# Kernel tuning notes

Hardware: AMD Instinct MI355X
Metric: run time of the kernel (lower is better)

The kernel has to match this reference:

```python
import math
import jax, jax.numpy as jnp
import numpy as np

N, NFEAT, NHID, NCLASS, NLAYERS = 8192, 500, 128, 40, 4
ALPHA, GAMMA, LAMBDA, MAX_W = 0.1, 0.1, 0.5, 0.05


def _col_stochastic(w):
    # Uniform(0,1) -> clamp to [0, MAX_W] -> column normalize (ColumnStochasticGraphConvolution init)
    w = jnp.clip(w, 0.0, MAX_W)
    return w / jnp.clip(w.sum(axis=0, keepdims=True), 1e-8, None)


def setup_inputs() -> dict:
    key = jax.random.key(0)
    ks = jax.random.split(key, 10)
    x = jax.random.normal(ks[0], (N, NFEAT), dtype=jnp.float32)
    adj = (jax.random.uniform(ks[1], (N, N)) < 0.002).astype(jnp.float32)
    s_in = 1.0 / math.sqrt(NFEAT)
    fc_in_w = jax.random.uniform(ks[2], (NFEAT, NHID), minval=-s_in, maxval=s_in, dtype=jnp.float32)
    fc_in_b = jnp.zeros((NHID,), jnp.float32)
    c = jax.random.normal(ks[3], (NHID,), dtype=jnp.float32)
    s_h = 1.0 / math.sqrt(NHID)
    w_gcnii = jax.random.uniform(ks[4], (NLAYERS, NHID, NHID), minval=-s_h, maxval=s_h, dtype=jnp.float32)
    b_gcnii = jax.random.uniform(ks[5], (NLAYERS, NHID), minval=-s_h, maxval=s_h, dtype=jnp.float32)
    w_lin = jax.vmap(_col_stochastic)(jax.random.uniform(ks[6], (NLAYERS, NHID, NHID), dtype=jnp.float32))
    b_lin = jnp.zeros((NLAYERS, NHID), jnp.float32)
    fc_out_w = jax.random.uniform(ks[7], (NHID, NCLASS), minval=-s_h, maxval=s_h, dtype=jnp.float32)
    fc_out_b = jnp.zeros((NCLASS,), jnp.float32)
    return {"x": x, "adj": adj, "fc_in_w": fc_in_w, "fc_in_b": fc_in_b, "c": c,
            "w_gcnii": w_gcnii, "b_gcnii": b_gcnii, "w_lin": w_lin, "b_lin": b_lin,
            "fc_out_w": fc_out_w, "fc_out_b": fc_out_b}


def _normalize_adj(adj):
    # A_hat = D^{-1/2} (A + I) D^{-1/2}
    a = adj + jnp.eye(adj.shape[0], dtype=adj.dtype)
    deg = a.sum(axis=1)
    dinv = jnp.where(deg > 0, jax.lax.rsqrt(deg), 0.0)
    return dinv[:, None] * a * dinv[None, :]


def reference(x, adj, fc_in_w, fc_in_b, c, w_gcnii, b_gcnii, w_lin, b_lin, fc_out_w, fc_out_b):
    a_hat = _normalize_adj(adj)                      # [N, N]
    h = jax.nn.relu(x @ fc_in_w + fc_in_b)           # [N, nhid]
    h = (1.0 - GAMMA) * h + GAMMA * c[None, :]       # H0 preconditioning with learnable c
    h0 = h
    # dropout is identity in eval mode
    for i in range(NLAYERS):
        beta = math.log(LAMBDA / (i + 1) + 1.0)
        # linear propagation branch: A_hat @ (H W'_i) + b'_i  (column-stochastic W')
        linear_part = a_hat @ (h @ w_lin[i]) + b_lin[i]
        # GCNII branch: sigma(((1-a) A_hat H + a H0)((1-b) I + b W_i)) + b_i
        support = (1.0 - ALPHA) * (a_hat @ h) + ALPHA * h0
        gcnii = jax.nn.relu((1.0 - beta) * support + beta * (support @ w_gcnii[i]) + b_gcnii[i])
        h = linear_part + gcnii
    return h @ fc_out_w + fc_out_b                   # [N, nclass] logits
```

## Files before the change

### kernel.cpp

```cpp
#include <hip/hip_runtime.h>
#include <math.h>

#define NROWS 8192
#define NFEATD 500
#define NHID 128
#define NCLS 40
#define CAP 64
#define FCIN_BLOCKS (NROWS / 8)
#define CSR_BLOCKS  (NROWS / 4)
#define ROWS_PB 8

typedef float f32x4 __attribute__((ext_vector_type(4)));
typedef float f32x2 __attribute__((ext_vector_type(2)));

__global__ __launch_bounds__(256) void k_pre(
    const float* __restrict__ x, const float* __restrict__ w,
    const float* __restrict__ b, const float* __restrict__ c,
    const float* __restrict__ adj,
    float* __restrict__ h, float* __restrict__ h0,
    float* __restrict__ dinv, int* __restrict__ cnts, int* __restrict__ cols)
{
    __shared__ float xs[8][504];
    int tid = threadIdx.x;
    if (blockIdx.x < FCIN_BLOCKS) {
        int col = tid & 127;
        int rg = tid >> 7;
        int r0 = blockIdx.x * 8;
        for (int rr = 0; rr < 8; ++rr)
            for (int k = tid; k < NFEATD; k += 256)
                xs[rr][k] = x[(size_t)(r0 + rr) * NFEATD + k];
        __syncthreads();
        float bias = b[col];
        float acc[4] = {bias, bias, bias, bias};
        for (int k4 = 0; k4 < NFEATD / 4; ++k4) {
            int k = k4 * 4;
            f32x4 a0 = *(const f32x4*)&xs[rg * 4 + 0][k];
            f32x4 a1 = *(const f32x4*)&xs[rg * 4 + 1][k];
            f32x4 a2 = *(const f32x4*)&xs[rg * 4 + 2][k];
            f32x4 a3 = *(const f32x4*)&xs[rg * 4 + 3][k];
            float w0 = w[(k + 0) * NHID + col];
            float w1 = w[(k + 1) * NHID + col];
            float w2 = w[(k + 2) * NHID + col];
            float w3 = w[(k + 3) * NHID + col];
            acc[0] += a0.x * w0 + a0.y * w1 + a0.z * w2 + a0.w * w3;
            acc[1] += a1.x * w0 + a1.y * w1 + a1.z * w2 + a1.w * w3;
            acc[2] += a2.x * w0 + a2.y * w1 + a2.z * w2 + a2.w * w3;
            acc[3] += a3.x * w0 + a3.y * w1 + a3.z * w2 + a3.w * w3;
        }
        float cv = c[col];
#pragma unroll
        for (int rr = 0; rr < 4; ++rr) {
            float hv = 0.9f * fmaxf(acc[rr], 0.0f) + 0.1f * cv;
            size_t o = (size_t)(r0 + rg * 4 + rr) * NHID + col;
            h[o] = hv;
            h0[o] = hv;
        }
    } else {
        int bid = blockIdx.x - FCIN_BLOCKS;
        int r = bid * 4 + (tid >> 6);
        int lane = tid & 63;
        const f32x4* row4 = (const f32x4*)(adj + (size_t)r * NROWS);
        int* mycols = cols + (size_t)r * CAP;
        unsigned long long lt = (1ull << lane) - 1ull;
        int cnt = 0;
        for (int it = 0; it < NROWS / 256; ++it) {
            f32x4 v = __builtin_nontemporal_load(&row4[it * 64 + lane]);
            int base = it * 256 + 4 * lane;
            bool nz; unsigned long long m;
            nz = (v.x != 0.0f); m = __ballot(nz);
            if (nz) { int p = cnt + __popcll(m & lt); mycols[p < CAP ? p : CAP - 1] = base; }
            cnt += __popcll(m);
            nz = (v.y != 0.0f); m = __ballot(nz);
            if (nz) { int p = cnt + __popcll(m & lt); mycols[p < CAP ? p : CAP - 1] = base + 1; }
            cnt += __popcll(m);
            nz = (v.z != 0.0f); m = __ballot(nz);
            if (nz) { int p = cnt + __popcll(m & lt); mycols[p < CAP ? p : CAP - 1] = base + 2; }
            cnt += __popcll(m);
            nz = (v.w != 0.0f); m = __ballot(nz);
            if (nz) { int p = cnt + __popcll(m & lt); mycols[p < CAP ? p : CAP - 1] = base + 3; }
            cnt += __popcll(m);
        }
        if (lane == 0) {
            cnts[r] = cnt < CAP ? cnt : CAP;
            dinv[r] = rsqrtf((float)cnt + 1.0f);
        }
    }
}

__global__ __launch_bounds__(256) void k_scale(
    const float* __restrict__ h, const float* __restrict__ dinv,
    float* __restrict__ ht)
{
    int gid = blockIdx.x * 256 + threadIdx.x;
    float2 v = ((const float2*)h)[gid];
    float d = dinv[gid >> 6];
    ((float2*)ht)[gid] = make_float2(v.x * d, v.y * d);
}

__global__ __launch_bounds__(256) void k_layer(
    const float* __restrict__ ht, const float* __restrict__ h0,
    const float* __restrict__ dinv, const int* __restrict__ cnts,
    const int* __restrict__ cols,
    const float* __restrict__ wlin, const float* __restrict__ blin,
    const float* __restrict__ wg, const float* __restrict__ bg,
    float beta, float* __restrict__ htout,
    const float* __restrict__ fow, const float* __restrict__ fob,
    float* __restrict__ out, int final_layer)
{
    __shared__ float ahs[ROWS_PB][NHID];
    __shared__ float ss[ROWS_PB][NHID];
    __shared__ float red[2][ROWS_PB][NHID];
    int tid = threadIdx.x;
    int lane = tid & 63;
    int wid = tid >> 6;
    int r0 = blockIdx.x * ROWS_PB;
    const float2* ht2 = (const float2*)ht;
    const float2* h02 = (const float2*)h0;

    for (int rr = 2 * wid; rr < 2 * wid + 2; ++rr) {
        int r = r0 + rr;
        int n = cnts[r];
        const int* mc = cols + (size_t)r * CAP;
        float ax = 0.f, ay = 0.f;
        int e = 0;
        for (; e + 4 <= n; e += 4) {
            int j0 = mc[e], j1 = mc[e + 1], j2 = mc[e + 2], j3 = mc[e + 3];
            float2 v0 = ht2[(size_t)j0 * 64 + lane];
            float2 v1 = ht2[(size_t)j1 * 64 + lane];
            float2 v2 = ht2[(size_t)j2 * 64 + lane];
            float2 v3 = ht2[(size_t)j3 * 64 + lane];
            ax += v0.x + v1.x + v2.x + v3.x;
            ay += v0.y + v1.y + v2.y + v3.y;
        }
        for (; e < n; ++e) {
            int j = mc[e];
            float2 v = ht2[(size_t)j * 64 + lane];
            ax += v.x;
            ay += v.y;
        }
        float di = dinv[r];
        float2 ti = ht2[(size_t)r * 64 + lane];
        float gx = di * (ax + ti.x);
        float gy = di * (ay + ti.y);
        float2 h0v = h02[(size_t)r * 64 + lane];
        ((float2*)&ahs[rr][0])[lane] = make_float2(gx, gy);
        ((float2*)&ss[rr][0])[lane] =
            make_float2(0.9f * gx + 0.1f * h0v.x, 0.9f * gy + 0.1f * h0v.y);
    }
    __syncthreads();

    int br = tid >> 7;
    int kh = (tid >> 6) & 1;
    int cp = tid & 63;
    const float* wmat = br ? wg : wlin;
    const float (*amat)[NHID] = br ? ss : ahs;
    f32x2 acc[8] = {{0,0},{0,0},{0,0},{0,0},{0,0},{0,0},{0,0},{0,0}};
    int kbase = kh * 64;
    for (int k4 = 0; k4 < 16; ++k4) {
        int k = kbase + 4 * k4;
        f32x4 a0 = *(const f32x4*)&amat[0][k];
        f32x4 a1 = *(const f32x4*)&amat[1][k];
        f32x4 a2 = *(const f32x4*)&amat[2][k];
        f32x4 a3 = *(const f32x4*)&amat[3][k];
        f32x4 a4 = *(const f32x4*)&amat[4][k];
        f32x4 a5 = *(const f32x4*)&amat[5][k];
        f32x4 a6 = *(const f32x4*)&amat[6][k];
        f32x4 a7 = *(const f32x4*)&amat[7][k];
        f32x2 w0 = ((const f32x2*)&wmat[(size_t)(k + 0) * NHID])[cp];
        f32x2 w1 = ((const f32x2*)&wmat[(size_t)(k + 1) * NHID])[cp];
        f32x2 w2 = ((const f32x2*)&wmat[(size_t)(k + 2) * NHID])[cp];
        f32x2 w3 = ((const f32x2*)&wmat[(size_t)(k + 3) * NHID])[cp];
        acc[0] += a0.x * w0 + a0.y * w1 + a0.z * w2 + a0.w * w3;
        acc[1] += a1.x * w0 + a1.y * w1 + a1.z * w2 + a1.w * w3;
        acc[2] += a2.x * w0 + a2.y * w1 + a2.z * w2 + a2.w * w3;
        acc[3] += a3.x * w0 + a3.y * w1 + a3.z * w2 + a3.w * w3;
        acc[4] += a4.x * w0 + a4.y * w1 + a4.z * w2 + a4.w * w3;
        acc[5] += a5.x * w0 + a5.y * w1 + a5.z * w2 + a5.w * w3;
        acc[6] += a6.x * w0 + a6.y * w1 + a6.z * w2 + a6.w * w3;
        acc[7] += a7.x * w0 + a7.y * w1 + a7.z * w2 + a7.w * w3;
    }

    if (kh == 1) {
#pragma unroll
        for (int rr = 0; rr < 8; ++rr)
            ((f32x2*)&red[br][rr][0])[cp] = acc[rr];
    }
    __syncthreads();
    if (kh == 0) {
#pragma unroll
        for (int rr = 0; rr < 8; ++rr)
            acc[rr] += ((const f32x2*)&red[br][rr][0])[cp];
    }
    f32x2 gv[8];
    if (br == 1 && kh == 0) {
        f32x2 bgv = ((const f32x2*)bg)[cp];
        float omb = 1.0f - beta;
#pragma unroll
        for (int rr = 0; rr < 8; ++rr) {
            f32x2 sv = ((const f32x2*)&ss[rr][0])[cp];
            f32x2 t = omb * sv + beta * acc[rr] + bgv;
            gv[rr].x = fmaxf(t.x, 0.f);
            gv[rr].y = fmaxf(t.y, 0.f);
        }
    }
    __syncthreads();
    if (br == 1 && kh == 0) {
#pragma unroll
        for (int rr = 0; rr < 8; ++rr)
            ((f32x2*)&red[0][rr][0])[cp] = gv[rr];
    }
    __syncthreads();

    if (!final_layer) {
        if (br == 0 && kh == 0) {
            f32x2 blv = ((const f32x2*)blin)[cp];
#pragma unroll
            for (int rr = 0; rr < 8; ++rr) {
                int row = r0 + rr;
                f32x2 g = ((const f32x2*)&red[0][rr][0])[cp];
                f32x2 o = acc[rr] + blv + g;
                ((f32x2*)htout)[(size_t)row * 64 + cp] = dinv[row] * o;
            }
        }
    } else {
        if (br == 0 && kh == 0) {
            f32x2 blv = ((const f32x2*)blin)[cp];
#pragma unroll
            for (int rr = 0; rr < 8; ++rr) {
                f32x2 g = ((const f32x2*)&red[0][rr][0])[cp];
                ((f32x2*)&ss[rr][0])[cp] = acc[rr] + blv + g;
            }
        }
        __syncthreads();
        int rr2 = tid >> 6, c2 = tid & 63;
        if (c2 < NCLS) {
#pragma unroll
            for (int half = 0; half < 2; ++half) {
                int lr = half * 4 + rr2;
                float a = fob[c2];
                for (int k = 0; k < NHID; ++k)
                    a += ss[lr][k] * fow[k * NCLS + c2];
                out[(size_t)(r0 + lr) * NCLS + c2] = a;
            }
        }
    }
}

extern "C" void kernel_launch(void* const* d_in, const int* in_sizes, int n_in,
                              void* d_out, int out_size, void* d_ws, size_t ws_size,
                              hipStream_t stream) {
    const float* x        = (const float*)d_in[0];
    const float* adj      = (const float*)d_in[1];
    const float* fc_in_w  = (const float*)d_in[2];
    const float* fc_in_b  = (const float*)d_in[3];
    const float* c        = (const float*)d_in[4];
    const float* w_gcnii  = (const float*)d_in[5];
    const float* b_gcnii  = (const float*)d_in[6];
    const float* w_lin    = (const float*)d_in[7];
    const float* b_lin    = (const float*)d_in[8];
    const float* fc_out_w = (const float*)d_in[9];
    const float* fc_out_b = (const float*)d_in[10];
    float* out = (float*)d_out;

    char* ws = (char*)d_ws;
    size_t off = 0;
    auto alloc = [&](size_t bytes) -> void* {
        void* p = ws + off;
        off += (bytes + 255) & ~(size_t)255;
        return p;
    };
    float* dinv = (float*)alloc((size_t)NROWS * 4);
    int*   cnts = (int*)  alloc((size_t)NROWS * 4);
    int*   cols = (int*)  alloc((size_t)NROWS * CAP * 4);
    float* hA   = (float*)alloc((size_t)NROWS * NHID * 4);
    float* h0   = (float*)alloc((size_t)NROWS * NHID * 4);
    float* htA  = (float*)alloc((size_t)NROWS * NHID * 4);
    float* htB  = (float*)alloc((size_t)NROWS * NHID * 4);

    k_pre<<<FCIN_BLOCKS + CSR_BLOCKS, 256, 0, stream>>>(
        x, fc_in_w, fc_in_b, c, adj, hA, h0, dinv, cnts, cols);
    k_scale<<<NROWS * 64 / 256, 256, 0, stream>>>(hA, dinv, htA);

    float* htb[2] = {htA, htB};
    for (int i = 0; i < 4; ++i) {
        float beta = logf(0.5f / (float)(i + 1) + 1.0f);
        k_layer<<<NROWS / ROWS_PB, 256, 0, stream>>>(
            htb[i & 1], h0, dinv, cnts, cols,
            w_lin + (size_t)i * NHID * NHID, b_lin + (size_t)i * NHID,
            w_gcnii + (size_t)i * NHID * NHID, b_gcnii + (size_t)i * NHID,
            beta, htb[(i + 1) & 1],
            fc_out_w, fc_out_b, out, (i == 3) ? 1 : 0);
    }
}
```

Baseline: 186.2 us.

## Fuse dinv prescale into first layer and widen layer blocks to 512 threads

Removes the separate k_scale kernel. The first layer now applies dinv per edge while it gathers unscaled h, which drops one launch and one full read and write of the hidden matrix. The layer kernel moves to 512 threads, so each wave gathers a single row and the K dimension of the dense matmul is split four ways with a three-buffer shared-memory reduction. The cost is extra shared memory, more reduction work, and per-edge dinv loads in layer 0.

Result: slower. 198.8 us (+6.7%).

```diff
diff --git a/kernel.cpp b/kernel.cpp
--- a/kernel.cpp
+++ b/kernel.cpp
@@ -87,76 +87,91 @@
     }
 }
 
-__global__ __launch_bounds__(256) void k_scale(
-    const float* __restrict__ h, const float* __restrict__ dinv,
-    float* __restrict__ ht)
-{
-    int gid = blockIdx.x * 256 + threadIdx.x;
-    float2 v = ((const float2*)h)[gid];
-    float d = dinv[gid >> 6];
-    ((float2*)ht)[gid] = make_float2(v.x * d, v.y * d);
-}
-
-__global__ __launch_bounds__(256) void k_layer(
-    const float* __restrict__ ht, const float* __restrict__ h0,
+__global__ __launch_bounds__(512) void k_layer(
+    const float* __restrict__ hin, const float* __restrict__ h0,
     const float* __restrict__ dinv, const int* __restrict__ cnts,
     const int* __restrict__ cols,
     const float* __restrict__ wlin, const float* __restrict__ blin,
     const float* __restrict__ wg, const float* __restrict__ bg,
     float beta, float* __restrict__ htout,
     const float* __restrict__ fow, const float* __restrict__ fob,
-    float* __restrict__ out, int final_layer)
+    float* __restrict__ out, int edge_dinv, int final_layer)
 {
     __shared__ float ahs[ROWS_PB][NHID];
     __shared__ float ss[ROWS_PB][NHID];
-    __shared__ float red[2][ROWS_PB][NHID];
+    __shared__ float red[3][2][ROWS_PB][NHID];
     int tid = threadIdx.x;
     int lane = tid & 63;
     int wid = tid >> 6;
     int r0 = blockIdx.x * ROWS_PB;
-    const float2* ht2 = (const float2*)ht;
+    const float2* h2 = (const float2*)hin;
     const float2* h02 = (const float2*)h0;
 
-    for (int rr = 2 * wid; rr < 2 * wid + 2; ++rr) {
+    {
+        int rr = wid;
         int r = r0 + rr;
         int n = cnts[r];
         const int* mc = cols + (size_t)r * CAP;
         float ax = 0.f, ay = 0.f;
         int e = 0;
-        for (; e + 4 <= n; e += 4) {
-            int j0 = mc[e], j1 = mc[e + 1], j2 = mc[e + 2], j3 = mc[e + 3];
-            float2 v0 = ht2[(size_t)j0 * 64 + lane];
-            float2 v1 = ht2[(size_t)j1 * 64 + lane];
-            float2 v2 = ht2[(size_t)j2 * 64 + lane];
-            float2 v3 = ht2[(size_t)j3 * 64 + lane];
-            ax += v0.x + v1.x + v2.x + v3.x;
-            ay += v0.y + v1.y + v2.y + v3.y;
-        }
-        for (; e < n; ++e) {
-            int j = mc[e];
-            float2 v = ht2[(size_t)j * 64 + lane];
-            ax += v.x;
-            ay += v.y;
-        }
-        float di = dinv[r];
-        float2 ti = ht2[(size_t)r * 64 + lane];
-        float gx = di * (ax + ti.x);
-        float gy = di * (ay + ti.y);
+        if (edge_dinv) {
+            for (; e + 4 <= n; e += 4) {
+                int j0 = mc[e], j1 = mc[e + 1], j2 = mc[e + 2], j3 = mc[e + 3];
+                float d0 = dinv[j0], d1 = dinv[j1], d2 = dinv[j2], d3 = dinv[j3];
+                float2 v0 = h2[(size_t)j0 * 64 + lane];
+                float2 v1 = h2[(size_t)j1 * 64 + lane];
+                float2 v2 = h2[(size_t)j2 * 64 + lane];
+                float2 v3 = h2[(size_t)j3 * 64 + lane];
+                ax += d0 * v0.x + d1 * v1.x + d2 * v2.x + d3 * v3.x;
+                ay += d0 * v0.y + d1 * v1.y + d2 * v2.y + d3 * v3.y;
+            }
+            for (; e < n; ++e) {
+                int j = mc[e];
+                float dj = dinv[j];
+                float2 v = h2[(size_t)j * 64 + lane];
+                ax += dj * v.x;
+                ay += dj * v.y;
+            }
+            float di = dinv[r];
+            float2 vi = h2[(size_t)r * 64 + lane];
+            ax = di * (ax + di * vi.x);
+            ay = di * (ay + di * vi.y);
+        } else {
+            for (; e + 4 <= n; e += 4) {
+                int j0 = mc[e], j1 = mc[e + 1], j2 = mc[e + 2], j3 = mc[e + 3];
+                float2 v0 = h2[(size_t)j0 * 64 + lane];
+                float2 v1 = h2[(size_t)j1 * 64 + lane];
+                float2 v2 = h2[(size_t)j2 * 64 + lane];
+                float2 v3 = h2[(size_t)j3 * 64 + lane];
+                ax += v0.x + v1.x + v2.x + v3.x;
+                ay += v0.y + v1.y + v2.y + v3.y;
+            }
+            for (; e < n; ++e) {
+                int j = mc[e];
+                float2 v = h2[(size_t)j * 64 + lane];
+                ax += v.x;
+                ay += v.y;
+            }
+            float di = dinv[r];
+            float2 ti = h2[(size_t)r * 64 + lane];
+            ax = di * (ax + ti.x);
+            ay = di * (ay + ti.y);
+        }
         float2 h0v = h02[(size_t)r * 64 + lane];
-        ((float2*)&ahs[rr][0])[lane] = make_float2(gx, gy);
+        ((float2*)&ahs[rr][0])[lane] = make_float2(ax, ay);
         ((float2*)&ss[rr][0])[lane] =
-            make_float2(0.9f * gx + 0.1f * h0v.x, 0.9f * gy + 0.1f * h0v.y);
+            make_float2(0.9f * ax + 0.1f * h0v.x, 0.9f * ay + 0.1f * h0v.y);
     }
     __syncthreads();
 
-    int br = tid >> 7;
-    int kh = (tid >> 6) & 1;
+    int br = tid >> 8;
+    int kq = (tid >> 6) & 3;
     int cp = tid & 63;
     const float* wmat = br ? wg : wlin;
     const float (*amat)[NHID] = br ? ss : ahs;
     f32x2 acc[8] = {{0,0},{0,0},{0,0},{0,0},{0,0},{0,0},{0,0},{0,0}};
-    int kbase = kh * 64;
-    for (int k4 = 0; k4 < 16; ++k4) {
+    int kbase = kq * 32;
+    for (int k4 = 0; k4 < 8; ++k4) {
         int k = kbase + 4 * k4;
         f32x4 a0 = *(const f32x4*)&amat[0][k];
         f32x4 a1 = *(const f32x4*)&amat[1][k];
@@ -180,19 +195,23 @@
         acc[7] += a7.x * w0 + a7.y * w1 + a7.z * w2 + a7.w * w3;
     }
 
-    if (kh == 1) {
+    if (kq != 0) {
 #pragma unroll
         for (int rr = 0; rr < 8; ++rr)
-            ((f32x2*)&red[br][rr][0])[cp] = acc[rr];
+            ((f32x2*)&red[kq - 1][br][rr][0])[cp] = acc[rr];
     }
     __syncthreads();
-    if (kh == 0) {
-#pragma unroll
-        for (int rr = 0; rr < 8; ++rr)
-            acc[rr] += ((const f32x2*)&red[br][rr][0])[cp];
+    if (kq == 0) {
+#pragma unroll
+        for (int rr = 0; rr < 8; ++rr) {
+            f32x2 p0 = ((const f32x2*)&red[0][br][rr][0])[cp];
+            f32x2 p1 = ((const f32x2*)&red[1][br][rr][0])[cp];
+            f32x2 p2 = ((const f32x2*)&red[2][br][rr][0])[cp];
+            acc[rr] += p0 + p1 + p2;
+        }
     }
     f32x2 gv[8];
-    if (br == 1 && kh == 0) {
+    if (br == 1 && kq == 0) {
         f32x2 bgv = ((const f32x2*)bg)[cp];
         float omb = 1.0f - beta;
 #pragma unroll
@@ -204,44 +223,40 @@
         }
     }
     __syncthreads();
-    if (br == 1 && kh == 0) {
+    if (br == 1 && kq == 0) {
 #pragma unroll
         for (int rr = 0; rr < 8; ++rr)
-            ((f32x2*)&red[0][rr][0])[cp] = gv[rr];
+            ((f32x2*)&red[0][0][rr][0])[cp] = gv[rr];
     }
     __syncthreads();
 
     if (!final_layer) {
-        if (br == 0 && kh == 0) {
+        if (br == 0 && kq == 0) {
             f32x2 blv = ((const f32x2*)blin)[cp];
 #pragma unroll
             for (int rr = 0; rr < 8; ++rr) {
                 int row = r0 + rr;
-                f32x2 g = ((const f32x2*)&red[0][rr][0])[cp];
+                f32x2 g = ((const f32x2*)&red[0][0][rr][0])[cp];
                 f32x2 o = acc[rr] + blv + g;
                 ((f32x2*)htout)[(size_t)row * 64 + cp] = dinv[row] * o;
             }
         }
     } else {
-        if (br == 0 && kh == 0) {
+        if (br == 0 && kq == 0) {
             f32x2 blv = ((const f32x2*)blin)[cp];
 #pragma unroll
             for (int rr = 0; rr < 8; ++rr) {
-                f32x2 g = ((const f32x2*)&red[0][rr][0])[cp];
+                f32x2 g = ((const f32x2*)&red[0][0][rr][0])[cp];
                 ((f32x2*)&ss[rr][0])[cp] = acc[rr] + blv + g;
             }
         }
         __syncthreads();
         int rr2 = tid >> 6, c2 = tid & 63;
         if (c2 < NCLS) {
-#pragma unroll
-            for (int half = 0; half < 2; ++half) {
-                int lr = half * 4 + rr2;
-                float a = fob[c2];
-                for (int k = 0; k < NHID; ++k)
-                    a += ss[lr][k] * fow[k * NCLS + c2];
-                out[(size_t)(r0 + lr) * NCLS + c2] = a;
-            }
+            float a = fob[c2];
+            for (int k = 0; k < NHID; ++k)
+                a += ss[rr2][k] * fow[k * NCLS + c2];
+            out[(size_t)(r0 + rr2) * NCLS + c2] = a;
         }
     }
 }
@@ -279,16 +294,16 @@
 
     k_pre<<<FCIN_BLOCKS + CSR_BLOCKS, 256, 0, stream>>>(
         x, fc_in_w, fc_in_b, c, adj, hA, h0, dinv, cnts, cols);
-    k_scale<<<NROWS * 64 / 256, 256, 0, stream>>>(hA, dinv, htA);
-
-    float* htb[2] = {htA, htB};
+
+    const float* hin[4] = {hA, htA, htB, htA};
+    float* hout[4]      = {htA, htB, htA, nullptr};
     for (int i = 0; i < 4; ++i) {
         float beta = logf(0.5f / (float)(i + 1) + 1.0f);
-        k_layer<<<NROWS / ROWS_PB, 256, 0, stream>>>(
-            htb[i & 1], h0, dinv, cnts, cols,
+        k_layer<<<NROWS / ROWS_PB, 512, 0, stream>>>(
+            hin[i], h0, dinv, cnts, cols,
             w_lin + (size_t)i * NHID * NHID, b_lin + (size_t)i * NHID,
             w_gcnii + (size_t)i * NHID * NHID, b_gcnii + (size_t)i * NHID,
-            beta, htb[(i + 1) & 1],
-            fc_out_w, fc_out_b, out, (i == 3) ? 1 : 0);
+            beta, hout[i], fc_out_w, fc_out_b, out,
+            (i == 0) ? 1 : 0, (i == 3) ? 1 : 0);
     }
 }
```
